# Kernel optimization log

Measured on AMD Instinct MI355X. Metric: run time of the kernel, lower is better.

The kernel has to match this reference:

```python
import jax, jax.numpy as jnp
import numpy as np

NUM_HEADS = 16


def _rotate_half(x):
    x1, x2 = jnp.split(x, 2, axis=-1)
    return jnp.concatenate([-x2, x1], axis=-1)


def _rope_apply(x, sin, cos):
    return x * cos + _rotate_half(x) * sin


def setup_inputs() -> dict:
    key = jax.random.key(0)
    ks = jax.random.split(key, 6)
    B, N, C, HD = 2, 2048, 1024, 64
    x = jax.random.normal(ks[0], (B, N, C), dtype=jnp.float32)
    sin = jax.random.uniform(ks[1], (N - 1, HD), dtype=jnp.float32)
    cos = jax.random.uniform(ks[2], (N - 1, HD), dtype=jnp.float32)
    qkv_w = jax.random.normal(ks[3], (3 * C, C), dtype=jnp.float32) * (C ** -0.5)
    proj_w = jax.random.normal(ks[4], (C, C), dtype=jnp.float32) * (C ** -0.5)
    proj_b = jax.random.normal(ks[5], (C,), dtype=jnp.float32) * 0.02
    return {"x": x, "sin": sin, "cos": cos, "qkv_w": qkv_w,
            "proj_w": proj_w, "proj_b": proj_b}


def reference(x, sin, cos, qkv_w, proj_w, proj_b):
    B, N, C = x.shape
    H = NUM_HEADS
    hd = C // H
    scale = hd ** -0.5

    # QKV projection (no bias): [B,N,3C] -> [B,N,3,H,hd]
    qkv = jnp.einsum('bnc,dc->bnd', x, qkv_w).reshape(B, N, 3, H, hd)
    q = qkv[:, :, 0].transpose(0, 2, 1, 3)  # [B,H,N,hd]
    k = qkv[:, :, 1].transpose(0, 2, 1, 3)
    v = qkv[:, :, 2].transpose(0, 2, 1, 3)

    # RoPE with prefix tokens left unrotated
    prefix = N - sin.shape[0]
    q = jnp.concatenate([q[:, :, :prefix], _rope_apply(q[:, :, prefix:], sin, cos)], axis=2)
    k = jnp.concatenate([k[:, :, :prefix], _rope_apply(k[:, :, prefix:], sin, cos)], axis=2)

    # SDPA (non-causal, no mask)
    scores = jnp.einsum('bhqd,bhkd->bhqk', q, k) * scale
    attn = jax.nn.softmax(scores, axis=-1)
    o = jnp.einsum('bhqk,bhkd->bhqd', attn, v)  # [B,H,N,hd]
    o = o.transpose(0, 2, 1, 3).reshape(B, N, C)

    # Output projection
    return jnp.einsum('bnc,dc->bnd', o, proj_w) + proj_b
```

## Files before the change

kernel.cpp:

```cpp
#include <hip/hip_runtime.h>
#include <hip/hip_bf16.h>
#include <stdint.h>

typedef __hip_bfloat16 bf16;
typedef __attribute__((ext_vector_type(8))) short short8;
typedef __attribute__((ext_vector_type(4))) float floatx4;

#define DEVI static __device__ __forceinline__

typedef __attribute__((address_space(1))) const uint32_t gu32;
typedef __attribute__((address_space(3))) uint32_t lu32;

DEVI void gld_lds16(const void* g, void* l) {
    __builtin_amdgcn_global_load_lds((gu32*)g, (lu32*)l, 16, 0, 0);
}

#define ROPE_N (2 * 2047 * 2 * 16 * 32)

#define QSCALE 0.18033688011112042f
#define SM_SHIFT 16.0f

__global__ void cvt_bf16_kernel(const float* __restrict__ src, bf16* __restrict__ dst, int n) {
    int i = (blockIdx.x * 256 + threadIdx.x) * 4;
    if (i >= n) return;
    float4 v = *(const float4*)(src + i);
    union { bf16 h[4]; uint2 u; } o;
    o.h[0] = __float2bfloat16(v.x);
    o.h[1] = __float2bfloat16(v.y);
    o.h[2] = __float2bfloat16(v.z);
    o.h[3] = __float2bfloat16(v.w);
    *(uint2*)(dst + i) = o.u;
}

template<int OUT_BF16, int ADD_BIAS, int SCALE_Q>
__global__ __launch_bounds__(256, 2) void gemm_bt_kernel(
    const bf16* __restrict__ A, const bf16* __restrict__ Bt,
    const float* __restrict__ bias, void* __restrict__ Cout,
    int M, int N, int K, int nbn)
{
    constexpr int BK = 32;
    __shared__ __align__(16) bf16 As[128 * BK];
    __shared__ __align__(16) bf16 Bs[128 * BK];
    const int sb = (blockIdx.x & 7) * ((int)gridDim.x >> 3) + (blockIdx.x >> 3);
    const int bm = sb / nbn;
    const int bn = sb % nbn;
    const int lane = threadIdx.x & 63;
    const int wave = threadIdx.x >> 6;
    const int wm = (wave >> 1) << 6;
    const int wn = (wave & 1) << 6;

    const int srow0 = wave * 16 + (lane >> 2);
    const int srow1 = srow0 + 64;
    const int skc = (lane & 3) * 8;
    const bf16* Ap0 = A + (size_t)(bm * 128 + srow0) * K + skc;
    const bf16* Ap1 = A + (size_t)(bm * 128 + srow1) * K + skc;
    const bf16* Bp0 = Bt + (size_t)(bn * 128 + srow0) * K + skc;
    const bf16* Bp1 = Bt + (size_t)(bn * 128 + srow1) * K + skc;
    bf16* As0 = &As[wave * 512];
    bf16* As1 = &As[wave * 512 + 2048];
    bf16* Bs0 = &Bs[wave * 512];
    bf16* Bs1 = &Bs[wave * 512 + 2048];

    const int frow = lane & 15;
    const int fk   = (lane >> 4) * 8;

    floatx4 acc[4][4] = {};

    for (int kt = 0; kt < K; kt += BK) {
        gld_lds16(Ap0 + kt, As0);
        gld_lds16(Ap1 + kt, As1);
        gld_lds16(Bp0 + kt, Bs0);
        gld_lds16(Bp1 + kt, Bs1);
        __syncthreads();
        short8 af[4], bfv[4];
#pragma unroll
        for (int m = 0; m < 4; ++m) af[m] = *(const short8*)&As[(wm + m * 16 + frow) * BK + fk];
#pragma unroll
        for (int n = 0; n < 4; ++n) bfv[n] = *(const short8*)&Bs[(wn + n * 16 + frow) * BK + fk];
#pragma unroll
        for (int m = 0; m < 4; ++m)
#pragma unroll
            for (int n = 0; n < 4; ++n)
                acc[m][n] = __builtin_amdgcn_mfma_f32_16x16x32_bf16(af[m], bfv[n], acc[m][n], 0, 0, 0);
        __syncthreads();
    }

    const int rbase = bm * 128 + wm + (lane >> 4) * 4;
    const int cbase = bn * 128 + wn + (lane & 15);
#pragma unroll
    for (int m = 0; m < 4; ++m)
#pragma unroll
        for (int n = 0; n < 4; ++n) {
            const int col = cbase + n * 16;
            float bv = ADD_BIAS ? bias[col] : 0.f;
            const float qs = (SCALE_Q && col < 1024) ? QSCALE : 1.0f;
#pragma unroll
            for (int r = 0; r < 4; ++r) {
                const size_t idx = (size_t)(rbase + m * 16 + r) * N + col;
                float v = acc[m][n][r] * qs + bv;
                if (OUT_BF16) ((bf16*)Cout)[idx] = __float2bfloat16(v);
                else          ((float*)Cout)[idx] = v;
            }
        }
}

__global__ void rope_kernel(bf16* __restrict__ qkv, const float* __restrict__ sinp,
                            const float* __restrict__ cosp) {
    int idx = blockIdx.x * 256 + threadIdx.x;
    if (idx >= ROPE_N) return;
    const int j = idx & 31;
    int t = idx >> 5;
    const int h = t & 15; t >>= 4;
    const int w = t & 1;  t >>= 1;
    const int n1 = t % 2047;
    const int b  = t / 2047;
    const size_t off = (size_t)(b * 2048 + n1 + 1) * 3072 + w * 1024 + h * 64 + j;
    const float x1 = __bfloat162float(qkv[off]);
    const float x2 = __bfloat162float(qkv[off + 32]);
    const int sc = n1 * 64 + j;
    const float c1 = cosp[sc], s1 = sinp[sc];
    const float c2 = cosp[sc + 32], s2 = sinp[sc + 32];
    qkv[off]      = __float2bfloat16(x1 * c1 - x2 * s1);
    qkv[off + 32] = __float2bfloat16(x2 * c2 + x1 * s2);
}

__global__ __launch_bounds__(512, 4) void attn_kernel(const bf16* __restrict__ qkv,
                                                      bf16* __restrict__ O) {
    __shared__ __align__(16) bf16 Ks[2][64 * 64];
    __shared__ __align__(16) bf16 Vt[2][64 * 64];

    const int bid = blockIdx.x;
    const int bh = bid & 31;
    const int qt = bid >> 5;
    const int b = bh >> 4;
    const int h = bh & 15;
    const int lane = threadIdx.x & 63;
    const int wave = threadIdx.x >> 6;
    const int t = threadIdx.x;

    const bf16* qb = qkv + (size_t)b * 2048 * 3072 + h * 64;
    const bf16* kb = qb + 1024;
    const bf16* vb = qb + 2048;

    const int frow = lane & 15;
    const int ks   = lane >> 4;
    const int q0   = qt * 128 + wave * 16;

    const bf16* qr = qb + (size_t)(q0 + frow) * 3072;
    const short8 qf0 = *(const short8*)(qr + ks * 8);
    const short8 qf1 = *(const short8*)(qr + 32 + ks * 8);

    short8 vfo = {};
    if (frow == 0) {
        const short one = (short)0x3F80;
#pragma unroll
        for (int j = 0; j < 8; ++j) vfo[j] = one;
    }

    const bool vrole = (wave < 4);

    const int kidx = (wave & 3) * 64 + lane;
    const int kr0 = kidx >> 3, kr1 = (kidx + 256) >> 3;
    const bf16* Kp0 = kb + (size_t)kr0 * 3072 + (((kidx & 7) ^ (kr0 & 7)) * 8);
    const bf16* Kp1 = kb + (size_t)kr1 * 3072 + (((kidx & 7) ^ (kr1 & 7)) * 8);

    const int vkt = wave & 3;
    const int vg  = (t >> 4) & 3;
    const int cb  = t & 15;
    const bf16* Vp = vb + (size_t)(vkt * 16 + vg * 4) * 3072 + cb * 4;
    const int vc = vg + ((vkt >> 1) << 2);
    const int vr = (vkt & 1) * 4;

    floatx4 acc[4] = {};
    floatx4 acc_s = {};

    union VU { ushort4 v; unsigned short e[4]; };
    VU vv[4];

    auto stage_issue = [&](int k0, int buf) {
        if (vrole) {
#pragma unroll
            for (int i = 0; i < 4; ++i)
                vv[i].v = *(const ushort4*)(Vp + (size_t)(k0 + i) * 3072);
        } else {
            gld_lds16(Kp0 + (size_t)k0 * 3072, &Ks[buf][(wave & 3) * 512]);
            gld_lds16(Kp1 + (size_t)k0 * 3072, &Ks[buf][(wave & 3) * 512 + 2048]);
        }
    };
    auto stage_write = [&](int buf) {
        if (vrole) {
#pragma unroll
            for (int j = 0; j < 4; ++j) {
                union { unsigned short u[4]; unsigned long long ll; } pk;
#pragma unroll
                for (int i = 0; i < 4; ++i) pk.u[i] = vv[i].e[j];
                const int d = cb * 4 + j;
                const int s = ((d >> 2) & 7) ^ ((d & 3) << 1);
                *(unsigned long long*)&Vt[buf][d * 64 + (((vc ^ s) << 3) + vr)] = pk.ll;
            }
        }
    };

    stage_issue(0, 0);
    stage_write(0);
    __syncthreads();

    for (int tt = 0; tt < 32; ++tt) {
        const int cur = tt & 1;
        if (tt < 31) stage_issue((tt + 1) * 64, cur ^ 1);

        short8 kf0[4], kf1[4];
#pragma unroll
        for (int kt = 0; kt < 4; ++kt) {
            const int row = kt * 16 + frow;
            kf0[kt] = *(const short8*)&Ks[cur][row * 64 + ((ks ^ (row & 7)) * 8)];
            kf1[kt] = *(const short8*)&Ks[cur][row * 64 + (((ks + 4) ^ (row & 7)) * 8)];
        }
        short8 vf0[4], vf1[4];
#pragma unroll
        for (int dt = 0; dt < 4; ++dt) {
            const int d = dt * 16 + frow;
            const int s = ((d >> 2) & 7) ^ ((d & 3) << 1);
            vf0[dt] = *(const short8*)&Vt[cur][d * 64 + ((ks ^ s) << 3)];
            vf1[dt] = *(const short8*)&Vt[cur][d * 64 + (((ks + 4) ^ s) << 3)];
        }

        floatx4 sv[4];
        __builtin_amdgcn_s_setprio(1);
#pragma unroll
        for (int kt = 0; kt < 4; ++kt) {
            floatx4 z = {-SM_SHIFT, -SM_SHIFT, -SM_SHIFT, -SM_SHIFT};
            z = __builtin_amdgcn_mfma_f32_16x16x32_bf16(kf0[kt], qf0, z, 0, 0, 0);
            z = __builtin_amdgcn_mfma_f32_16x16x32_bf16(kf1[kt], qf1, z, 0, 0, 0);
            sv[kt] = z;
        }
        __builtin_amdgcn_s_setprio(0);

        union PU { __hip_bfloat162 h2[4]; short8 v; };
        PU p0, p1;
#pragma unroll
        for (int kt = 0; kt < 4; ++kt)
#pragma unroll
            for (int m = 0; m < 2; ++m) {
                const float a = __builtin_amdgcn_exp2f(sv[kt][2 * m]);
                const float c = __builtin_amdgcn_exp2f(sv[kt][2 * m + 1]);
                const __hip_bfloat162 pk = __float22bfloat162_rn(float2{a, c});
                if (kt < 2) p0.h2[kt * 2 + m] = pk;
                else        p1.h2[(kt - 2) * 2 + m] = pk;
            }

        __builtin_amdgcn_s_setprio(1);
#pragma unroll
        for (int dt = 0; dt < 4; ++dt) {
            acc[dt] = __builtin_amdgcn_mfma_f32_16x16x32_bf16(p0.v, vf0[dt], acc[dt], 0, 0, 0);
            acc[dt] = __builtin_amdgcn_mfma_f32_16x16x32_bf16(p1.v, vf1[dt], acc[dt], 0, 0, 0);
        }
        acc_s = __builtin_amdgcn_mfma_f32_16x16x32_bf16(p0.v, vfo, acc_s, 0, 0, 0);
        acc_s = __builtin_amdgcn_mfma_f32_16x16x32_bf16(p1.v, vfo, acc_s, 0, 0, 0);
        __builtin_amdgcn_s_setprio(0);

        if (tt < 31) stage_write(cur ^ 1);
        __syncthreads();
    }

    floatx4 li;
#pragma unroll
    for (int i = 0; i < 4; ++i) li[i] = 1.0f / __shfl(acc_s[i], lane & 48);
    const int nrow = q0 + (lane >> 4) * 4;
#pragma unroll
    for (int i = 0; i < 4; ++i) {
        const size_t base = ((size_t)b * 2048 + nrow + i) * 1024 + h * 64 + frow;
#pragma unroll
        for (int dt = 0; dt < 4; ++dt)
            O[base + dt * 16] = __float2bfloat16(acc[dt][i] * li[i]);
    }
}

extern "C" void kernel_launch(void* const* d_in, const int* in_sizes, int n_in,
                              void* d_out, int out_size, void* d_ws, size_t ws_size,
                              hipStream_t stream) {
    const float* x      = (const float*)d_in[0];
    const float* sinp   = (const float*)d_in[1];
    const float* cosp   = (const float*)d_in[2];
    const float* qkv_w  = (const float*)d_in[3];
    const float* proj_w = (const float*)d_in[4];
    const float* proj_b = (const float*)d_in[5];
    float* out = (float*)d_out;

    char* ws = (char*)d_ws;
    bf16* xb    = (bf16*)(ws);
    bf16* wqkv  = (bf16*)(ws + 8388608);
    bf16* wproj = (bf16*)(ws + 8388608 + 6291456);
    bf16* qkvb  = (bf16*)(ws + 16777216);
    bf16* attno = (bf16*)(ws + 16777216 + 25165824);

    cvt_bf16_kernel<<<4096, 256, 0, stream>>>(x, xb, 4194304);
    cvt_bf16_kernel<<<3072, 256, 0, stream>>>(qkv_w, wqkv, 3145728);
    cvt_bf16_kernel<<<1024, 256, 0, stream>>>(proj_w, wproj, 1048576);

    gemm_bt_kernel<1, 0, 1><<<32 * 24, 256, 0, stream>>>(xb, wqkv, nullptr, qkvb,
                                                         4096, 3072, 1024, 24);
    rope_kernel<<<(ROPE_N + 255) / 256, 256, 0, stream>>>(qkvb, sinp, cosp);
    attn_kernel<<<512, 512, 0, stream>>>(qkvb, attno);
    gemm_bt_kernel<0, 1, 0><<<32 * 8, 256, 0, stream>>>(attno, wproj, proj_b, out,
                                                        4096, 1024, 1024, 8);
}
```

Baseline: 129.4 us.

## Fuse RoPE into QKV GEMM epilogue, shrink proj GEMM tile, deepen attention pipeline

Applies RoPE (and the Q scale) inside the QKV GEMM epilogue, pairing accumulator fragments 32 columns apart, and drops the separate rope kernel with its read-modify-write of q/k. The output projection GEMM now uses 64-row tiles so it launches twice as many blocks, improving occupancy on a small grid. The attention kernel goes from two to four LDS buffers and processes two K/V tiles per barrier, halving syncs at the cost of more LDS and registers. The epilogue now also reads sin/cos from global memory per element, which adds scattered loads inside the GEMM.

New measurement: 130.5 us. Within noise of the previous version (+0.8%).

```diff
diff --git a/kernel.cpp b/kernel.cpp
--- a/kernel.cpp
+++ b/kernel.cpp
@@ -14,8 +14,6 @@
 DEVI void gld_lds16(const void* g, void* l) {
     __builtin_amdgcn_global_load_lds((gu32*)g, (lu32*)l, 16, 0, 0);
 }
-
-#define ROPE_N (2 * 2047 * 2 * 16 * 32)
 
 #define QSCALE 0.18033688011112042f
 #define SM_SHIFT 16.0f
@@ -32,30 +30,31 @@
     *(uint2*)(dst + i) = o.u;
 }
 
-template<int OUT_BF16, int ADD_BIAS, int SCALE_Q>
+template<int BM, int OUT_BF16, int ADD_BIAS, int SCALE_Q, int ROPE>
 __global__ __launch_bounds__(256, 2) void gemm_bt_kernel(
     const bf16* __restrict__ A, const bf16* __restrict__ Bt,
-    const float* __restrict__ bias, void* __restrict__ Cout,
+    const float* __restrict__ bias, const float* __restrict__ sinp,
+    const float* __restrict__ cosp, void* __restrict__ Cout,
     int M, int N, int K, int nbn)
 {
     constexpr int BK = 32;
-    __shared__ __align__(16) bf16 As[128 * BK];
+    constexpr int MFRAG = BM / 32;
+    __shared__ __align__(16) bf16 As[BM * BK];
     __shared__ __align__(16) bf16 Bs[128 * BK];
     const int sb = (blockIdx.x & 7) * ((int)gridDim.x >> 3) + (blockIdx.x >> 3);
     const int bm = sb / nbn;
     const int bn = sb % nbn;
     const int lane = threadIdx.x & 63;
     const int wave = threadIdx.x >> 6;
-    const int wm = (wave >> 1) << 6;
+    const int wm = (wave >> 1) * (BM / 2);
     const int wn = (wave & 1) << 6;
 
     const int srow0 = wave * 16 + (lane >> 2);
-    const int srow1 = srow0 + 64;
     const int skc = (lane & 3) * 8;
-    const bf16* Ap0 = A + (size_t)(bm * 128 + srow0) * K + skc;
-    const bf16* Ap1 = A + (size_t)(bm * 128 + srow1) * K + skc;
+    const bf16* Ap0 = A + (size_t)(bm * BM + srow0) * K + skc;
+    const bf16* Ap1 = A + (size_t)(bm * BM + srow0 + 64) * K + skc;
     const bf16* Bp0 = Bt + (size_t)(bn * 128 + srow0) * K + skc;
-    const bf16* Bp1 = Bt + (size_t)(bn * 128 + srow1) * K + skc;
+    const bf16* Bp1 = Bt + (size_t)(bn * 128 + srow0 + 64) * K + skc;
     bf16* As0 = &As[wave * 512];
     bf16* As1 = &As[wave * 512 + 2048];
     bf16* Bs0 = &Bs[wave * 512];
@@ -64,70 +63,74 @@
     const int frow = lane & 15;
     const int fk   = (lane >> 4) * 8;
 
-    floatx4 acc[4][4] = {};
+    floatx4 acc[MFRAG][4] = {};
 
     for (int kt = 0; kt < K; kt += BK) {
         gld_lds16(Ap0 + kt, As0);
-        gld_lds16(Ap1 + kt, As1);
+        if (BM == 128) gld_lds16(Ap1 + kt, As1);
         gld_lds16(Bp0 + kt, Bs0);
         gld_lds16(Bp1 + kt, Bs1);
         __syncthreads();
-        short8 af[4], bfv[4];
-#pragma unroll
-        for (int m = 0; m < 4; ++m) af[m] = *(const short8*)&As[(wm + m * 16 + frow) * BK + fk];
+        short8 af[MFRAG], bfv[4];
+#pragma unroll
+        for (int m = 0; m < MFRAG; ++m) af[m] = *(const short8*)&As[(wm + m * 16 + frow) * BK + fk];
 #pragma unroll
         for (int n = 0; n < 4; ++n) bfv[n] = *(const short8*)&Bs[(wn + n * 16 + frow) * BK + fk];
 #pragma unroll
-        for (int m = 0; m < 4; ++m)
+        for (int m = 0; m < MFRAG; ++m)
 #pragma unroll
             for (int n = 0; n < 4; ++n)
                 acc[m][n] = __builtin_amdgcn_mfma_f32_16x16x32_bf16(af[m], bfv[n], acc[m][n], 0, 0, 0);
         __syncthreads();
     }
 
-    const int rbase = bm * 128 + wm + (lane >> 4) * 4;
-    const int cbase = bn * 128 + wn + (lane & 15);
-#pragma unroll
-    for (int m = 0; m < 4; ++m)
-#pragma unroll
-        for (int n = 0; n < 4; ++n) {
-            const int col = cbase + n * 16;
-            float bv = ADD_BIAS ? bias[col] : 0.f;
-            const float qs = (SCALE_Q && col < 1024) ? QSCALE : 1.0f;
-#pragma unroll
-            for (int r = 0; r < 4; ++r) {
-                const size_t idx = (size_t)(rbase + m * 16 + r) * N + col;
-                float v = acc[m][n][r] * qs + bv;
-                if (OUT_BF16) ((bf16*)Cout)[idx] = __float2bfloat16(v);
-                else          ((float*)Cout)[idx] = v;
+    const int rbase = bm * BM + wm + (lane >> 4) * 4;
+    const int cbase = bn * 128 + wn + frow;
+#pragma unroll
+    for (int m = 0; m < MFRAG; ++m)
+#pragma unroll
+        for (int r = 0; r < 4; ++r) {
+            const int row = rbase + m * 16 + r;
+            if (ROPE) {
+                const int ntok = row & 2047;
+                const int n1 = ntok - 1;
+#pragma unroll
+                for (int p = 0; p < 2; ++p) {
+                    const int colA = cbase + p * 16;
+                    const float qs = (SCALE_Q && colA < 1024) ? QSCALE : 1.0f;
+                    float vA = acc[m][p][r] * qs;
+                    float vB = acc[m][p + 2][r] * qs;
+                    if (colA < 2048 && ntok >= 1) {
+                        const int j = colA & 63;
+                        const int sc = n1 * 64 + j;
+                        const float c1 = cosp[sc],      s1 = sinp[sc];
+                        const float c2 = cosp[sc + 32], s2 = sinp[sc + 32];
+                        const float oA = vA * c1 - vB * s1;
+                        const float oB = vB * c2 + vA * s2;
+                        vA = oA; vB = oB;
+                    }
+                    const size_t ia = (size_t)row * N + colA;
+                    ((bf16*)Cout)[ia]      = __float2bfloat16(vA);
+                    ((bf16*)Cout)[ia + 32] = __float2bfloat16(vB);
+                }
+            } else {
+#pragma unroll
+                for (int n = 0; n < 4; ++n) {
+                    const int col = cbase + n * 16;
+                    const float bv = ADD_BIAS ? bias[col] : 0.f;
+                    const float v = acc[m][n][r] + bv;
+                    const size_t idx = (size_t)row * N + col;
+                    if (OUT_BF16) ((bf16*)Cout)[idx] = __float2bfloat16(v);
+                    else          ((float*)Cout)[idx] = v;
+                }
             }
         }
-}
-
-__global__ void rope_kernel(bf16* __restrict__ qkv, const float* __restrict__ sinp,
-                            const float* __restrict__ cosp) {
-    int idx = blockIdx.x * 256 + threadIdx.x;
-    if (idx >= ROPE_N) return;
-    const int j = idx & 31;
-    int t = idx >> 5;
-    const int h = t & 15; t >>= 4;
-    const int w = t & 1;  t >>= 1;
-    const int n1 = t % 2047;
-    const int b  = t / 2047;
-    const size_t off = (size_t)(b * 2048 + n1 + 1) * 3072 + w * 1024 + h * 64 + j;
-    const float x1 = __bfloat162float(qkv[off]);
-    const float x2 = __bfloat162float(qkv[off + 32]);
-    const int sc = n1 * 64 + j;
-    const float c1 = cosp[sc], s1 = sinp[sc];
-    const float c2 = cosp[sc + 32], s2 = sinp[sc + 32];
-    qkv[off]      = __float2bfloat16(x1 * c1 - x2 * s1);
-    qkv[off + 32] = __float2bfloat16(x2 * c2 + x1 * s2);
 }
 
 __global__ __launch_bounds__(512, 4) void attn_kernel(const bf16* __restrict__ qkv,
                                                       bf16* __restrict__ O) {
-    __shared__ __align__(16) bf16 Ks[2][64 * 64];
-    __shared__ __align__(16) bf16 Vt[2][64 * 64];
+    __shared__ __align__(16) bf16 Ks[4][64 * 64];
+    __shared__ __align__(16) bf16 Vt[4][64 * 64];
 
     const int bid = blockIdx.x;
     const int bh = bid & 31;
@@ -175,54 +178,46 @@
     floatx4 acc_s = {};
 
     union VU { ushort4 v; unsigned short e[4]; };
-    VU vv[4];
-
-    auto stage_issue = [&](int k0, int buf) {
+    VU vv[2][4];
+
+    auto stage_issue = [&](int k0, int slot, int buf) {
         if (vrole) {
 #pragma unroll
             for (int i = 0; i < 4; ++i)
-                vv[i].v = *(const ushort4*)(Vp + (size_t)(k0 + i) * 3072);
+                vv[slot][i].v = *(const ushort4*)(Vp + (size_t)(k0 + i) * 3072);
         } else {
             gld_lds16(Kp0 + (size_t)k0 * 3072, &Ks[buf][(wave & 3) * 512]);
             gld_lds16(Kp1 + (size_t)k0 * 3072, &Ks[buf][(wave & 3) * 512 + 2048]);
         }
     };
-    auto stage_write = [&](int buf) {
+    auto stage_write = [&](int slot, int buf) {
         if (vrole) {
 #pragma unroll
             for (int j = 0; j < 4; ++j) {
                 union { unsigned short u[4]; unsigned long long ll; } pk;
 #pragma unroll
-                for (int i = 0; i < 4; ++i) pk.u[i] = vv[i].e[j];
+                for (int i = 0; i < 4; ++i) pk.u[i] = vv[slot][i].e[j];
                 const int d = cb * 4 + j;
                 const int s = ((d >> 2) & 7) ^ ((d & 3) << 1);
                 *(unsigned long long*)&Vt[buf][d * 64 + (((vc ^ s) << 3) + vr)] = pk.ll;
             }
         }
     };
-
-    stage_issue(0, 0);
-    stage_write(0);
-    __syncthreads();
-
-    for (int tt = 0; tt < 32; ++tt) {
-        const int cur = tt & 1;
-        if (tt < 31) stage_issue((tt + 1) * 64, cur ^ 1);
-
+    auto compute_tile = [&](int buf) {
         short8 kf0[4], kf1[4];
 #pragma unroll
         for (int kt = 0; kt < 4; ++kt) {
             const int row = kt * 16 + frow;
-            kf0[kt] = *(const short8*)&Ks[cur][row * 64 + ((ks ^ (row & 7)) * 8)];
-            kf1[kt] = *(const short8*)&Ks[cur][row * 64 + (((ks + 4) ^ (row & 7)) * 8)];
+            kf0[kt] = *(const short8*)&Ks[buf][row * 64 + ((ks ^ (row & 7)) * 8)];
+            kf1[kt] = *(const short8*)&Ks[buf][row * 64 + (((ks + 4) ^ (row & 7)) * 8)];
         }
         short8 vf0[4], vf1[4];
 #pragma unroll
         for (int dt = 0; dt < 4; ++dt) {
             const int d = dt * 16 + frow;
             const int s = ((d >> 2) & 7) ^ ((d & 3) << 1);
-            vf0[dt] = *(const short8*)&Vt[cur][d * 64 + ((ks ^ s) << 3)];
-            vf1[dt] = *(const short8*)&Vt[cur][d * 64 + (((ks + 4) ^ s) << 3)];
+            vf0[dt] = *(const short8*)&Vt[buf][d * 64 + ((ks ^ s) << 3)];
+            vf1[dt] = *(const short8*)&Vt[buf][d * 64 + (((ks + 4) ^ s) << 3)];
         }
 
         floatx4 sv[4];
@@ -258,8 +253,27 @@
         acc_s = __builtin_amdgcn_mfma_f32_16x16x32_bf16(p0.v, vfo, acc_s, 0, 0, 0);
         acc_s = __builtin_amdgcn_mfma_f32_16x16x32_bf16(p1.v, vfo, acc_s, 0, 0, 0);
         __builtin_amdgcn_s_setprio(0);
-
-        if (tt < 31) stage_write(cur ^ 1);
+    };
+
+    stage_issue(0, 0, 0);
+    stage_issue(64, 1, 1);
+    stage_write(0, 0);
+    stage_write(1, 1);
+    __syncthreads();
+
+    for (int tt = 0; tt < 32; tt += 2) {
+        const int b0 = tt & 3, b1 = (tt + 1) & 3;
+        const bool pf = (tt + 2) < 32;
+        if (pf) {
+            stage_issue((tt + 2) * 64, 0, (tt + 2) & 3);
+            stage_issue((tt + 3) * 64, 1, (tt + 3) & 3);
+        }
+        compute_tile(b0);
+        compute_tile(b1);
+        if (pf) {
+            stage_write(0, (tt + 2) & 3);
+            stage_write(1, (tt + 3) & 3);
+        }
         __syncthreads();
     }
 
@@ -298,10 +312,9 @@
     cvt_bf16_kernel<<<3072, 256, 0, stream>>>(qkv_w, wqkv, 3145728);
     cvt_bf16_kernel<<<1024, 256, 0, stream>>>(proj_w, wproj, 1048576);
 
-    gemm_bt_kernel<1, 0, 1><<<32 * 24, 256, 0, stream>>>(xb, wqkv, nullptr, qkvb,
-                                                         4096, 3072, 1024, 24);
-    rope_kernel<<<(ROPE_N + 255) / 256, 256, 0, stream>>>(qkvb, sinp, cosp);
+    gemm_bt_kernel<128, 1, 0, 1, 1><<<32 * 24, 256, 0, stream>>>(
+        xb, wqkv, nullptr, sinp, cosp, qkvb, 4096, 3072, 1024, 24);
     attn_kernel<<<512, 512, 0, stream>>>(qkvb, attno);
-    gemm_bt_kernel<0, 1, 0><<<32 * 8, 256, 0, stream>>>(attno, wproj, proj_b, out,
-                                                        4096, 1024, 1024, 8);
-}
+    gemm_bt_kernel<64, 0, 1, 0, 0><<<64 * 8, 256, 0, stream>>>(
+        attno, wproj, proj_b, nullptr, nullptr, out, 4096, 1024, 1024, 8);
+}
```
